# Performance work log

Hardware: AMD Instinct MI355X
Metric: run time of the kernel (lower is better)

The kernel has to match this reference:

```python
import jax, jax.numpy as jnp
import numpy as np

EPS = 1e-6
TTT_BASE_LR = 1.0
NUM_HEADS = 16


def _ln_fused_l2_bwd(x, l2_target, gamma, beta, eps=EPS):
    # Gradient of ||LN(x)*gamma+beta - target||^2/2 wrt x (fused LN + L2 bwd).
    mu = x.mean(axis=-1, keepdims=True)
    var = ((x - mu) ** 2).mean(axis=-1, keepdims=True)
    std = jnp.sqrt(var + eps)
    x_hat = (x - mu) / std
    grad_x_hat = (gamma * x_hat + beta - l2_target) * gamma
    z = (grad_x_hat
         - grad_x_hat.mean(axis=-1, keepdims=True)
         - x_hat * (grad_x_hat * x_hat).mean(axis=-1, keepdims=True)) / std
    return z


def _ln_fwd(x, gamma, beta, eps=EPS):
    mu = x.mean(axis=-1, keepdims=True)
    var = ((x - mu) ** 2).mean(axis=-1, keepdims=True)
    x_hat = (x - mu) / jnp.sqrt(var + eps)
    return gamma * x_hat + beta


def setup_inputs() -> dict:
    key = jax.random.key(0)
    ks = jax.random.split(key, 6)
    B, L, C, H = 2, 2048, 1024, NUM_HEADS
    D = C // H
    return {
        "hidden_states": jax.random.normal(ks[0], (B, L, C), jnp.float32),
        "Wq": jax.random.normal(ks[1], (C, C), jnp.float32) * 0.02,
        "Wk": jax.random.normal(ks[2], (C, C), jnp.float32) * 0.02,
        "Wv": jax.random.normal(ks[3], (C, C), jnp.float32) * 0.02,
        "W1": jax.random.normal(ks[4], (H, D, D), jnp.float32) * 0.02,
        "b1": jnp.zeros((H, 1, D), jnp.float32),
        "ttt_norm_weight": jnp.ones((H, D), jnp.float32),
        "ttt_norm_bias": jnp.zeros((H, D), jnp.float32),
        "lr_weight": jax.random.normal(ks[5], (H, C, 1), jnp.float32) * 0.02,
        "lr_bias": jnp.zeros((H, 1), jnp.float32),
    }


def reference(hidden_states, Wq, Wk, Wv, W1, b1,
              ttt_norm_weight, ttt_norm_bias, lr_weight, lr_bias):
    B, L, C = hidden_states.shape
    H = NUM_HEADS
    D = C // H

    def proj(W):  # nn.Linear(no bias): x @ W^T, then split heads -> [B,H,L,D]
        return (hidden_states @ W.T).reshape(B, L, H, D).transpose(0, 2, 1, 3)

    XQ, XK, XV = proj(Wq), proj(Wk), proj(Wv)

    # adaptive per-token learning rate eta: [B,H,L,1]
    ttt_lr = jnp.einsum("blc,hci->bhli", hidden_states, lr_weight)
    ttt_lr = jax.nn.sigmoid(ttt_lr + lr_bias.reshape(1, H, 1, 1))
    eta = TTT_BASE_LR * ttt_lr / D

    # inner-loop forward with initial fast weights W1,b1
    Z1 = jnp.einsum("bhld,hdf->bhlf", XK, W1) + b1[None]  # [B,H,L,D]
    recon_target = XV - XK

    gamma = ttt_norm_weight.reshape(1, H, 1, D)
    beta = ttt_norm_bias.reshape(1, H, 1, D)
    grad_l_wrt_Z1 = _ln_fused_l2_bwd(Z1, recon_target, gamma, beta)

    # dual form update (batch-parallel, no state carry)
    eg = eta * grad_l_wrt_Z1                               # [B,H,L,D]
    Attn1 = jnp.einsum("bhld,bhmd->bhlm", XQ, XK)          # [B,H,L,L]
    b1_bar = b1[None] - eg.sum(axis=2, keepdims=True)      # [B,H,1,D]
    Z1_bar = (jnp.einsum("bhld,hdf->bhlf", XQ, W1)
              - jnp.einsum("bhlm,bhmd->bhld", Attn1, eg)
              + b1_bar)

    Z1_normalized = _ln_fwd(Z1_bar, gamma, beta)
    return XQ + Z1_normalized  # [B,H,L,D]
```

## Files before the change

### kernel.cpp

```cpp
#include <hip/hip_runtime.h>
#include <math.h>

#define B_ 2
#define L_ 2048
#define C_ 1024
#define H_ 16
#define D_ 64
#define BH_ (B_*H_)
#define M_ (B_*L_)
#define N_ (3*C_)
#define K_ C_
#define EPS_ 1e-6f
#define NCHUNK_ 16
#define LDT_ 136
#define WTS_ 72

typedef unsigned short ushort_t;
typedef short short8 __attribute__((ext_vector_type(8)));
typedef float f32x4 __attribute__((ext_vector_type(4)));
typedef unsigned short ushort4_t __attribute__((ext_vector_type(4)));

__device__ __forceinline__ ushort_t f2bf(float f) {
    union { float f; unsigned u; } v; v.f = f;
    unsigned r = v.u + 0x7FFFu + ((v.u >> 16) & 1u);
    return (ushort_t)(r >> 16);
}
__device__ __forceinline__ float bf2f(ushort_t h) {
    union { unsigned u; float f; } v; v.u = ((unsigned)h) << 16;
    return v.f;
}

__device__ __forceinline__ void gload16(const void* g, void* l) {
    __builtin_amdgcn_global_load_lds(
        (const __attribute__((address_space(1))) void*)g,
        (__attribute__((address_space(3))) void*)l, 16, 0, 0);
}

__global__ __launch_bounds__(256) void cast_eta(
    const float* __restrict__ hs, const float* __restrict__ Wq,
    const float* __restrict__ Wk, const float* __restrict__ Wv,
    const float* __restrict__ W1, const float* __restrict__ lrw,
    const float* __restrict__ lrb, ushort_t* __restrict__ hsB,
    ushort_t* __restrict__ Wcat, float* __restrict__ eta,
    ushort_t* __restrict__ W1tg, float* __restrict__ W1tf) {
    __shared__ float pA[16][257], pB[16][257];
    const int bid = blockIdx.x, t = threadIdx.x;
    if (bid < 2048) {
        const int iA = bid * 2, iB = iA + 1;
        const float* rA = hs + (size_t)iA * C_;
        const float* rB = hs + (size_t)iB * C_;
        f32x4 a = *(const f32x4*)(rA + t * 4);
        f32x4 b = *(const f32x4*)(rB + t * 4);
        ushort4_t oa, ob;
        oa.x = f2bf(a.x); oa.y = f2bf(a.y); oa.z = f2bf(a.z); oa.w = f2bf(a.w);
        ob.x = f2bf(b.x); ob.y = f2bf(b.y); ob.z = f2bf(b.z); ob.w = f2bf(b.w);
        *(ushort4_t*)(hsB + (size_t)iA * C_ + t * 4) = oa;
        *(ushort4_t*)(hsB + (size_t)iB * C_ + t * 4) = ob;
        #pragma unroll
        for (int h = 0; h < 16; ++h) {
            f32x4 w = *(const f32x4*)(lrw + (size_t)h * C_ + t * 4);
            pA[h][t] = a.x * w.x + a.y * w.y + a.z * w.z + a.w * w.w;
            pB[h][t] = b.x * w.x + b.y * w.y + b.z * w.z + b.w * w.w;
        }
        __syncthreads();
        const int h = t >> 4, seg = t & 15;
        float sA = 0.f, sB = 0.f;
        #pragma unroll
        for (int j = 0; j < 16; ++j) {
            sA += pA[h][seg * 16 + j];
            sB += pB[h][seg * 16 + j];
        }
        #pragma unroll
        for (int m = 1; m < 16; m <<= 1) {
            sA += __shfl_xor(sA, m, 64);
            sB += __shfl_xor(sB, m, 64);
        }
        if (seg == 0) {
            float bb = lrb[h];
            int bA = iA >> 11, lA = iA & (L_ - 1);
            int bB = iB >> 11, lB = iB & (L_ - 1);
            eta[((size_t)(bA * H_ + h)) * L_ + lA] =
                (1.f / (1.f + expf(-(sA + bb)))) * (1.0f / 64.0f);
            eta[((size_t)(bB * H_ + h)) * L_ + lB] =
                (1.f / (1.f + expf(-(sB + bb)))) * (1.0f / 64.0f);
        }
    } else if (bid < 2816) {
        const int wb = bid - 2048;
        #pragma unroll
        for (int ii = 0; ii < 4; ++ii) {
            int cid = wb * 1024 + ii * 256 + t;
            int m = cid >> 18, r = cid & ((1 << 18) - 1);
            f32x4 v;
            if (m == 0)      v = *(const f32x4*)(Wq + (size_t)r * 4);
            else if (m == 1) v = *(const f32x4*)(Wk + (size_t)r * 4);
            else {
                f32x4 vv = *(const f32x4*)(Wv + (size_t)r * 4);
                f32x4 vk = *(const f32x4*)(Wk + (size_t)r * 4);
                v.x = vv.x - vk.x; v.y = vv.y - vk.y;
                v.z = vv.z - vk.z; v.w = vv.w - vk.w;
            }
            ushort4_t o;
            o.x = f2bf(v.x); o.y = f2bf(v.y); o.z = f2bf(v.z); o.w = f2bf(v.w);
            *(ushort4_t*)(Wcat + (size_t)m * (C_ * C_) + (size_t)r * 4) = o;
        }
    } else {
        const int h = bid - 2816;
        __shared__ float Wl[64 * 65];
        #pragma unroll
        for (int p = 0; p < 4; ++p) {
            int i4 = p * 256 + t;
            int e = i4 >> 4, f0 = (i4 & 15) * 4;
            f32x4 v = *(const f32x4*)(W1 + (size_t)h * 4096 + e * 64 + f0);
            Wl[(f0 + 0) * 65 + e] = v.x;
            Wl[(f0 + 1) * 65 + e] = v.y;
            Wl[(f0 + 2) * 65 + e] = v.z;
            Wl[(f0 + 3) * 65 + e] = v.w;
        }
        __syncthreads();
        #pragma unroll
        for (int p = 0; p < 16; ++p) {
            int flat = p * 256 + t;
            float v = Wl[(flat >> 6) * 65 + (flat & 63)];
            W1tf[(size_t)h * 4096 + flat] = v;
            W1tg[(size_t)h * 4096 + flat] = f2bf(v);
        }
    }
}

__global__ __launch_bounds__(256) void gemm_qkv(
    const ushort_t* __restrict__ A, const ushort_t* __restrict__ Bc,
    ushort_t* __restrict__ XQ, ushort_t* __restrict__ XK,
    ushort_t* __restrict__ XT) {
    __shared__ __align__(16) ushort_t smem[128 * 136];
    ushort_t* Al = smem;
    ushort_t* Bl = smem + 4096;
    const int bm = blockIdx.x, bn = blockIdx.y;
    const int t = threadIdx.x, w = t >> 6, lane = t & 63;
    const int wr = w >> 1, wc = w & 1;
    const int la15 = lane & 15, la4 = lane >> 4;
    f32x4 acc[4][4];
    #pragma unroll
    for (int a = 0; a < 4; a++)
        #pragma unroll
        for (int b = 0; b < 4; b++)
            #pragma unroll
            for (int j = 0; j < 4; j++) acc[a][b][j] = 0.f;

    const int ci0 = w * 64 + lane;
    const int xread = (la15 >> 1) & 3;
    const int uslot = la4 ^ xread;

    for (int kt = 0; kt < K_ / 32; ++kt) {
        __syncthreads();
        #pragma unroll
        for (int q = 0; q < 2; ++q) {
            int ci = q * 256 + ci0;
            int r = ci >> 2, kc = ci & 3;
            int kcp = kc ^ ((r >> 1) & 3);
            gload16(A + (size_t)(bm * 128 + r) * K_ + kt * 32 + kcp * 8,
                    &Al[q * 2048 + w * 512]);
            gload16(Bc + (size_t)(bn * 128 + r) * K_ + kt * 32 + kcp * 8,
                    &Bl[q * 2048 + w * 512]);
        }
        __syncthreads();
        short8 af[4], bfv[4];
        #pragma unroll
        for (int mf = 0; mf < 4; ++mf)
            af[mf] = *(const short8*)&Al[(wr * 64 + mf * 16 + la15) * 32 + uslot * 8];
        #pragma unroll
        for (int nf = 0; nf < 4; ++nf)
            bfv[nf] = *(const short8*)&Bl[(wc * 64 + nf * 16 + la15) * 32 + uslot * 8];
        #pragma unroll
        for (int mf = 0; mf < 4; ++mf)
            #pragma unroll
            for (int nf = 0; nf < 4; ++nf)
                acc[mf][nf] = __builtin_amdgcn_mfma_f32_16x16x32_bf16(
                    af[mf], bfv[nf], acc[mf][nf], 0, 0, 0);
    }

    __syncthreads();
    #pragma unroll
    for (int mf = 0; mf < 4; ++mf)
        #pragma unroll
        for (int nf = 0; nf < 4; ++nf)
            #pragma unroll
            for (int rg = 0; rg < 4; ++rg) {
                int i = wr * 64 + mf * 16 + la4 * 4 + rg;
                int j = wc * 64 + nf * 16 + la15;
                smem[i * 136 + j] = f2bf(acc[mf][nf][rg]);
            }
    __syncthreads();
    const int jbase = bn * 128;
    const int mtx = jbase >> 10;
    ushort_t* dst = (mtx == 0) ? XQ : (mtx == 1 ? XK : XT);
    const int hb = (jbase & 1023) >> 6;
    #pragma unroll
    for (int pass = 0; pass < 8; ++pass) {
        int i = pass * 16 + (t >> 4);
        int jj = (t & 15) * 8;
        short8 v = *(const short8*)&smem[i * 136 + jj];
        int ig = bm * 128 + i;
        int b = ig >> 11, l = ig & (L_ - 1);
        int h = hb + (jj >> 6), d = jj & 63;
        *(short8*)&dst[((size_t)(b * H_ + h) * L_ + l) * D_ + d] = v;
    }
}

__global__ __launch_bounds__(256) void k2_grad2(
    const ushort_t* __restrict__ XK, const ushort_t* __restrict__ XT,
    const ushort_t* __restrict__ W1tg, const float* __restrict__ b1,
    const float* __restrict__ tw, const float* __restrict__ tb,
    const float* __restrict__ eta, float* __restrict__ GpT,
    float* __restrict__ bsump) {
    __shared__ __align__(16) ushort_t xkt[64 * LDT_];
    __shared__ __align__(16) ushort_t egl[64 * LDT_];
    __shared__ float b1s[64], gs[64], bes[64];
    __shared__ float sred[4][64];
    const int bh = blockIdx.y, lt = blockIdx.x;
    const int h = bh & (H_ - 1);
    const int t = threadIdx.x, w = t >> 6, lane = t & 63;
    const int la15 = lane & 15, la4 = lane >> 4;
    if (t < 64) { b1s[t] = b1[h * 64 + t]; gs[t] = tw[h * 64 + t]; bes[t] = tb[h * 64 + t]; }
    __syncthreads();

    const ushort_t* xk = XK + (size_t)bh * L_ * D_;
    const ushort_t* xt = XT + (size_t)bh * L_ * D_;
    const ushort_t* w1g = W1tg + (size_t)h * 4096;
    const int l0 = lt * 128 + w * 32;
    const int llw = w * 32;

    f32x4 acc[2][4];
    #pragma unroll
    for (int mf = 0; mf < 2; mf++)
        #pragma unroll
        for (int nf = 0; nf < 4; nf++) {
            float bv = b1s[nf * 16 + la15];
            #pragma unroll
            for (int j = 0; j < 4; j++) acc[mf][nf][j] = bv;
        }
    #pragma unroll
    for (int ks = 0; ks < 2; ++ks) {
        short8 af[2], bfv[4];
        const int d0 = ks * 32 + la4 * 8;
        #pragma unroll
        for (int mf = 0; mf < 2; mf++) {
            af[mf] = *(const short8*)&xk[(size_t)(l0 + mf * 16 + la15) * D_ + d0];
            const int ll = llw + mf * 16 + la15;
            #pragma unroll
            for (int jj = 0; jj < 8; jj++)
                xkt[(d0 + jj) * LDT_ + ll] = (ushort_t)af[mf][jj];
        }
        #pragma unroll
        for (int nf = 0; nf < 4; nf++)
            bfv[nf] = *(const short8*)&w1g[(nf * 16 + la15) * 64 + d0];
        #pragma unroll
        for (int mf = 0; mf < 2; mf++)
            #pragma unroll
            for (int nf = 0; nf < 4; nf++)
                acc[mf][nf] = __builtin_amdgcn_mfma_f32_16x16x32_bf16(
                    af[mf], bfv[nf], acc[mf][nf], 0, 0, 0);
    }

    const float* etap = eta + (size_t)bh * L_;
    float accbs[4] = {0.f, 0.f, 0.f, 0.f};
    #pragma unroll
    for (int mf = 0; mf < 2; ++mf) {
        #pragma unroll
        for (int rg = 0; rg < 4; ++rg) {
            int lrow = l0 + mf * 16 + (la4 << 2) + rg;
            int llr  = llw + mf * 16 + (la4 << 2) + rg;
            float x[4], xh[4], gh[4];
            #pragma unroll
            for (int nf = 0; nf < 4; nf++) x[nf] = acc[mf][nf][rg];
            float s = x[0] + x[1] + x[2] + x[3];
            s += __shfl_xor(s, 1, 64); s += __shfl_xor(s, 2, 64);
            s += __shfl_xor(s, 4, 64); s += __shfl_xor(s, 8, 64);
            float mu = s * (1.f / 64.f);
            float vs = 0.f;
            #pragma unroll
            for (int nf = 0; nf < 4; nf++) { float dd = x[nf] - mu; vs += dd * dd; }
            vs += __shfl_xor(vs, 1, 64); vs += __shfl_xor(vs, 2, 64);
            vs += __shfl_xor(vs, 4, 64); vs += __shfl_xor(vs, 8, 64);
            float inv = 1.f / sqrtf(vs * (1.f / 64.f) + EPS_);
            float s1 = 0.f, s2 = 0.f;
            #pragma unroll
            for (int nf = 0; nf < 4; nf++) {
                int d = nf * 16 + la15;
                xh[nf] = (x[nf] - mu) * inv;
                float tgt = bf2f(xt[(size_t)lrow * D_ + d]);
                float g = gs[d];
                gh[nf] = (g * xh[nf] + bes[d] - tgt) * g;
                s1 += gh[nf]; s2 += gh[nf] * xh[nf];
            }
            s1 += __shfl_xor(s1, 1, 64); s1 += __shfl_xor(s1, 2, 64);
            s1 += __shfl_xor(s1, 4, 64); s1 += __shfl_xor(s1, 8, 64);
            s2 += __shfl_xor(s2, 1, 64); s2 += __shfl_xor(s2, 2, 64);
            s2 += __shfl_xor(s2, 4, 64); s2 += __shfl_xor(s2, 8, 64);
            float m1 = s1 * (1.f / 64.f), m2 = s2 * (1.f / 64.f);
            float el = etap[lrow];
            #pragma unroll
            for (int nf = 0; nf < 4; nf++) {
                int d = nf * 16 + la15;
                float egv = el * ((gh[nf] - m1 - xh[nf] * m2) * inv);
                accbs[nf] += egv;
                egl[d * LDT_ + llr] = f2bf(egv);
            }
        }
    }
    #pragma unroll
    for (int nf = 0; nf < 4; nf++) {
        accbs[nf] += __shfl_xor(accbs[nf], 16, 64);
        accbs[nf] += __shfl_xor(accbs[nf], 32, 64);
    }
    if (lane < 16)
        #pragma unroll
        for (int nf = 0; nf < 4; nf++) sred[w][nf * 16 + lane] = accbs[nf];
    __syncthreads();

    f32x4 aG[4];
    #pragma unroll
    for (int nf = 0; nf < 4; nf++)
        #pragma unroll
        for (int j = 0; j < 4; j++) aG[nf][j] = 0.f;
    #pragma unroll
    for (int ks = 0; ks < 4; ++ks) {
        const int ko = ks * 32 + la4 * 8;
        short8 ae = *(const short8*)&egl[(w * 16 + la15) * LDT_ + ko];
        #pragma unroll
        for (int nf = 0; nf < 4; nf++) {
            short8 be = *(const short8*)&xkt[(nf * 16 + la15) * LDT_ + ko];
            aG[nf] = __builtin_amdgcn_mfma_f32_16x16x32_bf16(ae, be, aG[nf], 0, 0, 0);
        }
    }
    float* gp = GpT + (size_t)(bh * NCHUNK_ + lt) * 4096;
    #pragma unroll
    for (int nf = 0; nf < 4; nf++)
        #pragma unroll
        for (int rg = 0; rg < 4; rg++) {
            int f = w * 16 + (la4 << 2) + rg;
            int e = nf * 16 + la15;
            gp[f * 64 + e] = aG[nf][rg];
        }
    if (t < 64)
        bsump[(bh * NCHUNK_ + lt) * 64 + t] =
            sred[0][t] + sred[1][t] + sred[2][t] + sred[3][t];
}

__global__ __launch_bounds__(256) void k3_out(
    const ushort_t* __restrict__ XQ, const float* __restrict__ W1tf,
    const float* __restrict__ GpT, const float* __restrict__ b1,
    const float* __restrict__ bsump, const float* __restrict__ tw,
    const float* __restrict__ tb, float* __restrict__ out) {
    __shared__ __align__(16) ushort_t Wt[64 * WTS_];
    __shared__ float b1s[64], gs[64], bes[64];
    const int bh = blockIdx.y, lt = blockIdx.x;
    const int h = bh & (H_ - 1);
    const int t = threadIdx.x, w = t >> 6, lane = t & 63;
    const int la15 = lane & 15, la4 = lane >> 4;
    for (int p = t; p < 4096; p += 256) {
        float s = W1tf[(size_t)h * 4096 + p];
        #pragma unroll
        for (int c = 0; c < NCHUNK_; c++)
            s -= GpT[(size_t)(bh * NCHUNK_ + c) * 4096 + p];
        Wt[(p >> 6) * WTS_ + (p & 63)] = f2bf(s);
    }
    if (t < 64) {
        float s = b1[h * 64 + t];
        #pragma unroll
        for (int c = 0; c < NCHUNK_; c++)
            s -= bsump[(bh * NCHUNK_ + c) * 64 + t];
        b1s[t] = s;
        gs[t] = tw[h * 64 + t]; bes[t] = tb[h * 64 + t];
    }
    __syncthreads();

    const ushort_t* xq = XQ + (size_t)bh * L_ * D_;
    const int l0 = lt * 128 + w * 32;
    f32x4 acc[2][4];
    #pragma unroll
    for (int mf = 0; mf < 2; mf++)
        #pragma unroll
        for (int nf = 0; nf < 4; nf++) {
            float bv = b1s[nf * 16 + la15];
            #pragma unroll
            for (int j = 0; j < 4; j++) acc[mf][nf][j] = bv;
        }
    #pragma unroll
    for (int ks = 0; ks < 2; ++ks) {
        short8 af[2], bfv[4];
        const int d0 = ks * 32 + la4 * 8;
        #pragma unroll
        for (int mf = 0; mf < 2; mf++)
            af[mf] = *(const short8*)&xq[(size_t)(l0 + mf * 16 + la15) * D_ + d0];
        #pragma unroll
        for (int nf = 0; nf < 4; nf++)
            bfv[nf] = *(const short8*)&Wt[(nf * 16 + la15) * WTS_ + d0];
        #pragma unroll
        for (int mf = 0; mf < 2; mf++)
            #pragma unroll
            for (int nf = 0; nf < 4; nf++)
                acc[mf][nf] = __builtin_amdgcn_mfma_f32_16x16x32_bf16(
                    af[mf], bfv[nf], acc[mf][nf], 0, 0, 0);
    }

    float* outp = out + (size_t)bh * L_ * D_;
    #pragma unroll
    for (int mf = 0; mf < 2; ++mf) {
        #pragma unroll
        for (int rg = 0; rg < 4; ++rg) {
            int lrow = l0 + mf * 16 + (la4 << 2) + rg;
            float x[4];
            #pragma unroll
            for (int nf = 0; nf < 4; nf++) x[nf] = acc[mf][nf][rg];
            float s = x[0] + x[1] + x[2] + x[3];
            s += __shfl_xor(s, 1, 64); s += __shfl_xor(s, 2, 64);
            s += __shfl_xor(s, 4, 64); s += __shfl_xor(s, 8, 64);
            float mu = s * (1.f / 64.f);
            float vs = 0.f;
            #pragma unroll
            for (int nf = 0; nf < 4; nf++) { float dd = x[nf] - mu; vs += dd * dd; }
            vs += __shfl_xor(vs, 1, 64); vs += __shfl_xor(vs, 2, 64);
            vs += __shfl_xor(vs, 4, 64); vs += __shfl_xor(vs, 8, 64);
            float inv = 1.f / sqrtf(vs * (1.f / 64.f) + EPS_);
            #pragma unroll
            for (int nf = 0; nf < 4; nf++) {
                int d = nf * 16 + la15;
                float xh = (x[nf] - mu) * inv;
                float o = gs[d] * xh + bes[d];
                float qv = bf2f(xq[(size_t)lrow * D_ + d]);
                outp[(size_t)lrow * D_ + d] = qv + o;
            }
        }
    }
}

extern "C" void kernel_launch(void* const* d_in, const int* in_sizes, int n_in,
                              void* d_out, int out_size, void* d_ws, size_t ws_size,
                              hipStream_t stream) {
    const float* hs  = (const float*)d_in[0];
    const float* Wq  = (const float*)d_in[1];
    const float* Wk  = (const float*)d_in[2];
    const float* Wv  = (const float*)d_in[3];
    const float* W1  = (const float*)d_in[4];
    const float* b1  = (const float*)d_in[5];
    const float* tw  = (const float*)d_in[6];
    const float* tb  = (const float*)d_in[7];
    const float* lrw = (const float*)d_in[8];
    const float* lrb = (const float*)d_in[9];
    float* out = (float*)d_out;

    char* ws = (char*)d_ws;
    size_t off = 0;
    ushort_t* hsB  = (ushort_t*)(ws + off); off += (size_t)M_ * K_ * 2;
    ushort_t* Wcat = (ushort_t*)(ws + off); off += (size_t)N_ * K_ * 2;
    ushort_t* XQ   = (ushort_t*)(ws + off); off += (size_t)M_ * C_ * 2;
    ushort_t* XK   = (ushort_t*)(ws + off); off += (size_t)M_ * C_ * 2;
    ushort_t* XT   = (ushort_t*)(ws + off); off += (size_t)M_ * C_ * 2;
    float*    eta  = (float*)(ws + off);    off += (size_t)BH_ * L_ * 4;
    ushort_t* W1tg = (ushort_t*)(ws + off); off += (size_t)H_ * D_ * D_ * 2;
    float*    W1tf = (float*)(ws + off);    off += (size_t)H_ * D_ * D_ * 4;
    float*    GpT   = (float*)hsB;
    float*    bsump = (float*)Wcat;

    cast_eta<<<2048 + 768 + 16, 256, 0, stream>>>(hs, Wq, Wk, Wv, W1, lrw, lrb,
                                                  hsB, Wcat, eta, W1tg, W1tf);
    gemm_qkv<<<dim3(M_ / 128, N_ / 128), 256, 0, stream>>>(hsB, Wcat, XQ, XK, XT);
    k2_grad2<<<dim3(L_ / 128, BH_), 256, 0, stream>>>(XK, XT, W1tg, b1, tw, tb, eta, GpT, bsump);
    k3_out<<<dim3(L_ / 128, BH_), 256, 0, stream>>>(XQ, W1tf, GpT, b1, bsump, tw, tb, out);
}
```

Before: 80.04 us.

## Load two K-tiles per barrier in QKV GEMM, add chunk-reduce kernel, single-pass LN stats

The QKV GEMM now loads two 32-wide K slices into separate shared buffers per barrier pair, halving the number of syncs and issuing more loads in flight. A new small kernel reduces the per-chunk partial gradients and bias sums once per head, instead of every k3_out block re-summing 16 partials. LayerNorm statistics in k2 and k3 are computed in one pass using sum and sum of squares with interleaved shuffles. The one-pass variance is less numerically stable, and the extra launch adds overhead.

```diff
diff --git a/kernel.cpp b/kernel.cpp
--- a/kernel.cpp
+++ b/kernel.cpp
@@ -132,8 +132,10 @@
     ushort_t* __restrict__ XQ, ushort_t* __restrict__ XK,
     ushort_t* __restrict__ XT) {
     __shared__ __align__(16) ushort_t smem[128 * 136];
-    ushort_t* Al = smem;
-    ushort_t* Bl = smem + 4096;
+    ushort_t* Al0 = smem;
+    ushort_t* Bl0 = smem + 4096;
+    ushort_t* Al1 = smem + 8192;
+    ushort_t* Bl1 = smem + 12288;
     const int bm = blockIdx.x, bn = blockIdx.y;
     const int t = threadIdx.x, w = t >> 6, lane = t & 63;
     const int wr = w >> 1, wc = w & 1;
@@ -149,34 +151,45 @@
     const int ci0 = w * 64 + lane;
     const int xread = (la15 >> 1) & 3;
     const int uslot = la4 ^ xread;
-
-    for (int kt = 0; kt < K_ / 32; ++kt) {
+    const int r0 = ci0 >> 2,         kcp0 = (ci0 & 3) ^ ((r0 >> 1) & 3);
+    const int r1 = (256 + ci0) >> 2, kcp1 = (ci0 & 3) ^ ((r1 >> 1) & 3);
+    const ushort_t* gA0 = A + (size_t)(bm * 128 + r0) * K_ + kcp0 * 8;
+    const ushort_t* gA1 = A + (size_t)(bm * 128 + r1) * K_ + kcp1 * 8;
+    const ushort_t* gB0 = Bc + (size_t)(bn * 128 + r0) * K_ + kcp0 * 8;
+    const ushort_t* gB1 = Bc + (size_t)(bn * 128 + r1) * K_ + kcp1 * 8;
+
+#define COMPUTE_T(AL, BL) do {                                              \
+        short8 af[4], bfv[4];                                               \
+        _Pragma("unroll")                                                   \
+        for (int mf = 0; mf < 4; ++mf)                                      \
+            af[mf] = *(const short8*)&(AL)[(wr * 64 + mf * 16 + la15) * 32 + uslot * 8]; \
+        _Pragma("unroll")                                                   \
+        for (int nf = 0; nf < 4; ++nf)                                      \
+            bfv[nf] = *(const short8*)&(BL)[(wc * 64 + nf * 16 + la15) * 32 + uslot * 8]; \
+        _Pragma("unroll")                                                   \
+        for (int mf = 0; mf < 4; ++mf)                                      \
+            _Pragma("unroll")                                               \
+            for (int nf = 0; nf < 4; ++nf)                                  \
+                acc[mf][nf] = __builtin_amdgcn_mfma_f32_16x16x32_bf16(      \
+                    af[mf], bfv[nf], acc[mf][nf], 0, 0, 0);                 \
+    } while (0)
+
+    for (int kt2 = 0; kt2 < 16; ++kt2) {
+        const int kA = kt2 * 64, kB = kA + 32;
         __syncthreads();
-        #pragma unroll
-        for (int q = 0; q < 2; ++q) {
-            int ci = q * 256 + ci0;
-            int r = ci >> 2, kc = ci & 3;
-            int kcp = kc ^ ((r >> 1) & 3);
-            gload16(A + (size_t)(bm * 128 + r) * K_ + kt * 32 + kcp * 8,
-                    &Al[q * 2048 + w * 512]);
-            gload16(Bc + (size_t)(bn * 128 + r) * K_ + kt * 32 + kcp * 8,
-                    &Bl[q * 2048 + w * 512]);
-        }
+        gload16(gA0 + kA, &Al0[w * 512]);
+        gload16(gB0 + kA, &Bl0[w * 512]);
+        gload16(gA1 + kA, &Al0[2048 + w * 512]);
+        gload16(gB1 + kA, &Bl0[2048 + w * 512]);
+        gload16(gA0 + kB, &Al1[w * 512]);
+        gload16(gB0 + kB, &Bl1[w * 512]);
+        gload16(gA1 + kB, &Al1[2048 + w * 512]);
+        gload16(gB1 + kB, &Bl1[2048 + w * 512]);
         __syncthreads();
-        short8 af[4], bfv[4];
-        #pragma unroll
-        for (int mf = 0; mf < 4; ++mf)
-            af[mf] = *(const short8*)&Al[(wr * 64 + mf * 16 + la15) * 32 + uslot * 8];
-        #pragma unroll
-        for (int nf = 0; nf < 4; ++nf)
-            bfv[nf] = *(const short8*)&Bl[(wc * 64 + nf * 16 + la15) * 32 + uslot * 8];
-        #pragma unroll
-        for (int mf = 0; mf < 4; ++mf)
-            #pragma unroll
-            for (int nf = 0; nf < 4; ++nf)
-                acc[mf][nf] = __builtin_amdgcn_mfma_f32_16x16x32_bf16(
-                    af[mf], bfv[nf], acc[mf][nf], 0, 0, 0);
-    }
+        COMPUTE_T(Al0, Bl0);
+        COMPUTE_T(Al1, Bl1);
+    }
+#undef COMPUTE_T
 
     __syncthreads();
     #pragma unroll
@@ -273,15 +286,14 @@
             #pragma unroll
             for (int nf = 0; nf < 4; nf++) x[nf] = acc[mf][nf][rg];
             float s = x[0] + x[1] + x[2] + x[3];
-            s += __shfl_xor(s, 1, 64); s += __shfl_xor(s, 2, 64);
-            s += __shfl_xor(s, 4, 64); s += __shfl_xor(s, 8, 64);
+            float q = x[0]*x[0] + x[1]*x[1] + x[2]*x[2] + x[3]*x[3];
+            s += __shfl_xor(s, 1, 64); q += __shfl_xor(q, 1, 64);
+            s += __shfl_xor(s, 2, 64); q += __shfl_xor(q, 2, 64);
+            s += __shfl_xor(s, 4, 64); q += __shfl_xor(q, 4, 64);
+            s += __shfl_xor(s, 8, 64); q += __shfl_xor(q, 8, 64);
             float mu = s * (1.f / 64.f);
-            float vs = 0.f;
-            #pragma unroll
-            for (int nf = 0; nf < 4; nf++) { float dd = x[nf] - mu; vs += dd * dd; }
-            vs += __shfl_xor(vs, 1, 64); vs += __shfl_xor(vs, 2, 64);
-            vs += __shfl_xor(vs, 4, 64); vs += __shfl_xor(vs, 8, 64);
-            float inv = 1.f / sqrtf(vs * (1.f / 64.f) + EPS_);
+            float var = q * (1.f / 64.f) - mu * mu;
+            float inv = 1.f / sqrtf(var + EPS_);
             float s1 = 0.f, s2 = 0.f;
             #pragma unroll
             for (int nf = 0; nf < 4; nf++) {
@@ -292,10 +304,10 @@
                 gh[nf] = (g * xh[nf] + bes[d] - tgt) * g;
                 s1 += gh[nf]; s2 += gh[nf] * xh[nf];
             }
-            s1 += __shfl_xor(s1, 1, 64); s1 += __shfl_xor(s1, 2, 64);
-            s1 += __shfl_xor(s1, 4, 64); s1 += __shfl_xor(s1, 8, 64);
-            s2 += __shfl_xor(s2, 1, 64); s2 += __shfl_xor(s2, 2, 64);
-            s2 += __shfl_xor(s2, 4, 64); s2 += __shfl_xor(s2, 8, 64);
+            s1 += __shfl_xor(s1, 1, 64); s2 += __shfl_xor(s2, 1, 64);
+            s1 += __shfl_xor(s1, 2, 64); s2 += __shfl_xor(s2, 2, 64);
+            s1 += __shfl_xor(s1, 4, 64); s2 += __shfl_xor(s2, 4, 64);
+            s1 += __shfl_xor(s1, 8, 64); s2 += __shfl_xor(s2, 8, 64);
             float m1 = s1 * (1.f / 64.f), m2 = s2 * (1.f / 64.f);
             float el = etap[lrow];
             #pragma unroll
@@ -346,10 +358,33 @@
             sred[0][t] + sred[1][t] + sred[2][t] + sred[3][t];
 }
 
+__global__ __launch_bounds__(256) void k2b_reduce(
+    const float* __restrict__ GpT, const float* __restrict__ bsump,
+    float* __restrict__ G, float* __restrict__ bsum) {
+    const int seg = blockIdx.x, bh = blockIdx.y;
+    const int t = threadIdx.x;
+    #pragma unroll 2
+    for (int ii = 0; ii < 2; ++ii) {
+        int i = seg * 512 + ii * 256 + t;
+        float s = 0.f;
+        #pragma unroll
+        for (int c = 0; c < NCHUNK_; c++)
+            s += GpT[(size_t)(bh * NCHUNK_ + c) * 4096 + i];
+        G[(size_t)bh * 4096 + i] = s;
+    }
+    if (seg == 0 && t < 64) {
+        float s = 0.f;
+        #pragma unroll
+        for (int c = 0; c < NCHUNK_; c++)
+            s += bsump[(bh * NCHUNK_ + c) * 64 + t];
+        bsum[bh * 64 + t] = s;
+    }
+}
+
 __global__ __launch_bounds__(256) void k3_out(
     const ushort_t* __restrict__ XQ, const float* __restrict__ W1tf,
-    const float* __restrict__ GpT, const float* __restrict__ b1,
-    const float* __restrict__ bsump, const float* __restrict__ tw,
+    const float* __restrict__ G, const float* __restrict__ b1,
+    const float* __restrict__ bsum, const float* __restrict__ tw,
     const float* __restrict__ tb, float* __restrict__ out) {
     __shared__ __align__(16) ushort_t Wt[64 * WTS_];
     __shared__ float b1s[64], gs[64], bes[64];
@@ -358,18 +393,11 @@
     const int t = threadIdx.x, w = t >> 6, lane = t & 63;
     const int la15 = lane & 15, la4 = lane >> 4;
     for (int p = t; p < 4096; p += 256) {
-        float s = W1tf[(size_t)h * 4096 + p];
-        #pragma unroll
-        for (int c = 0; c < NCHUNK_; c++)
-            s -= GpT[(size_t)(bh * NCHUNK_ + c) * 4096 + p];
+        float s = W1tf[(size_t)h * 4096 + p] - G[(size_t)bh * 4096 + p];
         Wt[(p >> 6) * WTS_ + (p & 63)] = f2bf(s);
     }
     if (t < 64) {
-        float s = b1[h * 64 + t];
-        #pragma unroll
-        for (int c = 0; c < NCHUNK_; c++)
-            s -= bsump[(bh * NCHUNK_ + c) * 64 + t];
-        b1s[t] = s;
+        b1s[t] = b1[h * 64 + t] - bsum[bh * 64 + t];
         gs[t] = tw[h * 64 + t]; bes[t] = tb[h * 64 + t];
     }
     __syncthreads();
@@ -413,15 +441,14 @@
             #pragma unroll
             for (int nf = 0; nf < 4; nf++) x[nf] = acc[mf][nf][rg];
             float s = x[0] + x[1] + x[2] + x[3];
-            s += __shfl_xor(s, 1, 64); s += __shfl_xor(s, 2, 64);
-            s += __shfl_xor(s, 4, 64); s += __shfl_xor(s, 8, 64);
+            float q = x[0]*x[0] + x[1]*x[1] + x[2]*x[2] + x[3]*x[3];
+            s += __shfl_xor(s, 1, 64); q += __shfl_xor(q, 1, 64);
+            s += __shfl_xor(s, 2, 64); q += __shfl_xor(q, 2, 64);
+            s += __shfl_xor(s, 4, 64); q += __shfl_xor(q, 4, 64);
+            s += __shfl_xor(s, 8, 64); q += __shfl_xor(q, 8, 64);
             float mu = s * (1.f / 64.f);
-            float vs = 0.f;
-            #pragma unroll
-            for (int nf = 0; nf < 4; nf++) { float dd = x[nf] - mu; vs += dd * dd; }
-            vs += __shfl_xor(vs, 1, 64); vs += __shfl_xor(vs, 2, 64);
-            vs += __shfl_xor(vs, 4, 64); vs += __shfl_xor(vs, 8, 64);
-            float inv = 1.f / sqrtf(vs * (1.f / 64.f) + EPS_);
+            float var = q * (1.f / 64.f) - mu * mu;
+            float inv = 1.f / sqrtf(var + EPS_);
             #pragma unroll
             for (int nf = 0; nf < 4; nf++) {
                 int d = nf * 16 + la15;
@@ -459,6 +486,8 @@
     float*    eta  = (float*)(ws + off);    off += (size_t)BH_ * L_ * 4;
     ushort_t* W1tg = (ushort_t*)(ws + off); off += (size_t)H_ * D_ * D_ * 2;
     float*    W1tf = (float*)(ws + off);    off += (size_t)H_ * D_ * D_ * 4;
+    float*    G    = (float*)(ws + off);    off += (size_t)BH_ * D_ * D_ * 4;
+    float*    bsum = (float*)(ws + off);    off += (size_t)BH_ * D_ * 4;
     float*    GpT   = (float*)hsB;
     float*    bsump = (float*)Wcat;
 
@@ -466,5 +495,6 @@
                                                   hsB, Wcat, eta, W1tg, W1tf);
     gemm_qkv<<<dim3(M_ / 128, N_ / 128), 256, 0, stream>>>(hsB, Wcat, XQ, XK, XT);
     k2_grad2<<<dim3(L_ / 128, BH_), 256, 0, stream>>>(XK, XT, W1tg, b1, tw, tb, eta, GpT, bsump);
-    k3_out<<<dim3(L_ / 128, BH_), 256, 0, stream>>>(XQ, W1tf, GpT, b1, bsump, tw, tb, out);
-}
+    k2b_reduce<<<dim3(8, BH_), 256, 0, stream>>>(GpT, bsump, G, bsum);
+    k3_out<<<dim3(L_ / 128, BH_), 256, 0, stream>>>(XQ, W1tf, G, b1, bsum, tw, tb, out);
+}
```

Result: no change. 78.94 us (-1.4%).
